# Optimization experiments

Hardware: AMD Instinct MI355X
Metric: run time of the kernel (lower is better)

Reference implementation:

```python
import jax, jax.numpy as jnp
import numpy as np

N, NS, D, HID = 8192, 512, 1024, 1024  # nodes, num_edges, f_dim, mlp hidden (max(f_dim,128))


def layernorm(x, g, b, eps=1e-5):
    m = x.mean(-1, keepdims=True)
    v = x.var(-1, keepdims=True)
    return (x - m) / jnp.sqrt(v + eps) * g + b


def mask_topk(a, kk):
    # keep only the top-kk entries of each row (vectorized version of mask_attn)
    _, idx = jax.lax.top_k(a, kk)
    rows = jnp.arange(a.shape[0])[:, None]
    mask = jnp.zeros(a.shape, a.dtype).at[rows, idx].set(1.0)
    return a * mask


def setup_inputs() -> dict:
    key = jax.random.key(0)
    ks = jax.random.split(key, 16)
    xavier = lambda k, i, o: jax.random.uniform(k, (i, o), jnp.float32, -1.0, 1.0) * np.sqrt(6.0 / (i + o))
    return {
        "inputs": jax.random.normal(ks[0], (N, D), jnp.float32),
        "noise": jax.random.normal(ks[1], (NS, D), jnp.float32),
        "edges_mu": jax.random.normal(ks[2], (1, D), jnp.float32),
        "edges_logsigma": xavier(ks[3], 1, D),
        "Wq": xavier(ks[4], D, D), "bq": jnp.zeros((D,), jnp.float32),
        "Wk": xavier(ks[5], D, D), "bk": jnp.zeros((D,), jnp.float32),
        "Wv": xavier(ks[6], D, D), "bv": jnp.zeros((D,), jnp.float32),
        "W1": xavier(ks[7], 2 * D, HID), "b1": jnp.zeros((HID,), jnp.float32),
        "W2": xavier(ks[8], HID, D), "b2": jnp.zeros((D,), jnp.float32),
        "g_in": jnp.ones((D,), jnp.float32), "b_in": jnp.zeros((D,), jnp.float32),
        "g_e": jnp.ones((D,), jnp.float32), "b_e": jnp.zeros((D,), jnp.float32),
        "k_n": 64,
        "k_e": 8,
    }


def reference(inputs, noise, edges_mu, edges_logsigma, Wq, bq, Wk, bk, Wv, bv,
              W1, b1, W2, b2, g_in, b_in, g_e, b_e, k_n, k_e):
    n, d = inputs.shape
    scale = d ** -0.5
    eps = 1e-8
    x = layernorm(inputs, g_in, b_in)                       # norm_input
    k = jax.nn.relu(x @ Wk + bk)                            # [N, D]
    v = jax.nn.relu(x @ Wv + bv)                            # [N, D]
    edges = edges_mu + jnp.exp(edges_logsigma) * noise      # [NS, D]
    # single iteration (iters=1)
    edges = layernorm(edges, g_e, b_e)                      # norm_edgs
    q = jax.nn.relu(edges @ Wq + bq)                        # [NS, D]
    dots = jnp.einsum('ni,mi->nm', q, k) * scale            # [NS, N]
    attn = jax.nn.softmax(dots, axis=1) + eps
    attn = attn / attn.sum(axis=1, keepdims=True)
    attn = mask_topk(attn, k_n)
    updates = jnp.einsum('nm,md->nd', attn, v)              # [NS, D]
    edges = jnp.concatenate([edges, updates], axis=1)       # [NS, 2D]
    edges = jax.nn.relu(edges @ W1 + b1) @ W2 + b2          # mlp -> [NS, D]
    q2 = x @ Wq + bq                                        # no relu in source
    k2 = jax.nn.relu(edges @ Wk + bk)                       # [NS, D]
    dots_v = jnp.einsum('ni,mi->nm', q2, k2) * scale        # [N, NS]
    attn_v = jax.nn.softmax(dots_v, axis=1)
    H = mask_topk(attn_v, k_e)
    return edges, H, dots
```

## Files before the change

### kernel.cpp

```cpp
#include <hip/hip_runtime.h>
#include <stdint.h>
#include <stddef.h>

typedef unsigned short u16;
typedef __bf16 bf16x8 __attribute__((ext_vector_type(8)));
typedef float f32x4 __attribute__((ext_vector_type(4)));

#define DEV __device__ __forceinline__

#define LSTR 40

DEV float bf2f(u16 u){ union{uint32_t i; float f;} c; c.i=(uint32_t)u<<16; return c.f; }
DEV u16 f2bf(float f){ union{float f; uint32_t i;} c; c.f=f; uint32_t x=c.i;
  uint32_t r = x + 0x7FFFu + ((x>>16)&1u); return (u16)(r>>16); }
DEV uint32_t fmap(float f){ union{float f; uint32_t u;} c; c.f=f;
  return (c.u & 0x80000000u) ? ~c.u : (c.u | 0x80000000u); }
DEV float funmap(uint32_t u){ union{uint32_t u; float f;} c;
  c.u = (u & 0x80000000u) ? (u & 0x7FFFFFFFu) : ~u; return c.f; }
DEV void split2(float x, u16& h, u16& l){ h = f2bf(x); l = f2bf(x - bf2f(h)); }

DEV float bredsum(float v, float* buf, int tid){
  #pragma unroll
  for(int o=32;o;o>>=1) v += __shfl_down(v,o);
  __syncthreads();
  if((tid&63)==0) buf[tid>>6]=v;
  __syncthreads();
  return buf[0]+buf[1]+buf[2]+buf[3];
}
DEV float bredmax(float v, float* buf, int tid){
  #pragma unroll
  for(int o=32;o;o>>=1) v = fmaxf(v, __shfl_down(v,o));
  __syncthreads();
  if((tid&63)==0) buf[tid>>6]=v;
  __syncthreads();
  return fmaxf(fmaxf(buf[0],buf[1]),fmaxf(buf[2],buf[3]));
}
DEV int bredsumi(int v, int* buf, int tid){
  #pragma unroll
  for(int o=32;o;o>>=1) v += __shfl_down(v,o);
  __syncthreads();
  if((tid&63)==0) buf[tid>>6]=v;
  __syncthreads();
  return buf[0]+buf[1]+buf[2]+buf[3];
}

template<bool RELU, int SK>
__global__ __launch_bounds__(256)
void gemm1_64(const u16* __restrict__ A, int lda,
              const u16* __restrict__ Bt, int ldb,
              const float* __restrict__ bias, float scale,
              u16* __restrict__ outb, float* __restrict__ outf,
              float* __restrict__ part,
              int K, int ldc, int M)
{
  __shared__ __align__(16) u16 As[64*LSTR];
  __shared__ __align__(16) u16 Bs[128*LSTR];
  const int tid = threadIdx.x, lane = tid&63, wave = tid>>6;
  const int m0 = blockIdx.y*64, n0 = blockIdx.x*128;
  const int wm = (wave>>1)*32, wn = (wave&1)*64;
  const int ml = lane&15, quad = lane>>4;
  const int srow = tid>>2, scol = (tid&3)*8;
  const int ks = K / SK;
  const int kbeg = blockIdx.z * ks;
  const u16* pa  = A  + (size_t)(m0+srow)*lda + kbeg + scol;
  const u16* pb0 = Bt + (size_t)(n0+srow)*ldb + kbeg + scol;
  const u16* pb1 = Bt + (size_t)(n0+64+srow)*ldb + kbeg + scol;

  f32x4 acc[2][4];
  #pragma unroll
  for(int i=0;i<2;i++)
    #pragma unroll
    for(int j=0;j<4;j++) acc[i][j] = (f32x4){0.f,0.f,0.f,0.f};

  uint4 ra=*(const uint4*)pa, rb0=*(const uint4*)pb0, rb1=*(const uint4*)pb1;
  for(int k0=0;k0<ks;k0+=32){
    __syncthreads();
    *(uint4*)&As[srow*LSTR + scol]      = ra;
    *(uint4*)&Bs[srow*LSTR + scol]      = rb0;
    *(uint4*)&Bs[(64+srow)*LSTR + scol] = rb1;
    __syncthreads();
    if(k0+32<ks){
      ra  = *(const uint4*)(pa +k0+32);
      rb0 = *(const uint4*)(pb0+k0+32);
      rb1 = *(const uint4*)(pb1+k0+32);
    }
    bf16x8 af[2], bf[4];
    #pragma unroll
    for(int mi=0;mi<2;mi++) af[mi] = *(const bf16x8*)&As[(wm+mi*16+ml)*LSTR + quad*8];
    #pragma unroll
    for(int ni=0;ni<4;ni++) bf[ni] = *(const bf16x8*)&Bs[(wn+ni*16+ml)*LSTR + quad*8];
    #pragma unroll
    for(int mi=0;mi<2;mi++)
      #pragma unroll
      for(int ni=0;ni<4;ni++)
        acc[mi][ni] = __builtin_amdgcn_mfma_f32_16x16x32_bf16(af[mi], bf[ni], acc[mi][ni], 0,0,0);
  }
  #pragma unroll
  for(int mi=0;mi<2;mi++){
    const int rbase = m0 + wm + mi*16 + quad*4;
    #pragma unroll
    for(int ni=0;ni<4;ni++){
      const int col = n0 + wn + ni*16 + ml;
      if(SK==1){
        const float bv = bias ? bias[col] : 0.f;
        #pragma unroll
        for(int r=0;r<4;r++){
          float v = acc[mi][ni][r]*scale + bv;
          if(RELU) v = fmaxf(v, 0.f);
          const size_t idx = (size_t)(rbase + r)*ldc + col;
          if(outb) outb[idx] = f2bf(v);
          if(outf) outf[idx] = v;
        }
      }else{
        #pragma unroll
        for(int r=0;r<4;r++)
          part[((size_t)blockIdx.z*M + rbase + r)*ldc + col] = acc[mi][ni][r];
      }
    }
  }
}

template<bool RELU, int SK>
__global__ __launch_bounds__(256)
void gemm3_64(const u16* __restrict__ Ah, const u16* __restrict__ Al, int lda,
              const u16* __restrict__ Bh, const u16* __restrict__ Bl, int ldb,
              const float* __restrict__ bias, float scale,
              u16* __restrict__ outh, u16* __restrict__ outl,
              float* __restrict__ outf, float* __restrict__ part,
              int K, int ldc, int M)
{
  __shared__ __align__(16) u16 AsH[64*LSTR];
  __shared__ __align__(16) u16 AsL[64*LSTR];
  __shared__ __align__(16) u16 BsH[128*LSTR];
  __shared__ __align__(16) u16 BsL[128*LSTR];
  const int tid = threadIdx.x, lane = tid&63, wave = tid>>6;
  const int m0 = blockIdx.y*64, n0 = blockIdx.x*128;
  const int wm = (wave>>1)*32, wn = (wave&1)*64;
  const int ml = lane&15, quad = lane>>4;
  const int srow = tid>>2, scol = (tid&3)*8;
  const int ks = K / SK;
  const int kbeg = blockIdx.z * ks;
  const size_t ao  = (size_t)(m0+srow)*lda + kbeg + scol;
  const size_t bo0 = (size_t)(n0+srow)*ldb + kbeg + scol;
  const size_t bo1 = (size_t)(n0+64+srow)*ldb + kbeg + scol;

  f32x4 acc[2][4];
  #pragma unroll
  for(int i=0;i<2;i++)
    #pragma unroll
    for(int j=0;j<4;j++) acc[i][j] = (f32x4){0.f,0.f,0.f,0.f};

  uint4 rah=*(const uint4*)(Ah+ao),  ral=*(const uint4*)(Al+ao);
  uint4 rbh0=*(const uint4*)(Bh+bo0), rbl0=*(const uint4*)(Bl+bo0);
  uint4 rbh1=*(const uint4*)(Bh+bo1), rbl1=*(const uint4*)(Bl+bo1);
  for(int k0=0;k0<ks;k0+=32){
    __syncthreads();
    *(uint4*)&AsH[srow*LSTR + scol]      = rah;
    *(uint4*)&AsL[srow*LSTR + scol]      = ral;
    *(uint4*)&BsH[srow*LSTR + scol]      = rbh0;
    *(uint4*)&BsL[srow*LSTR + scol]      = rbl0;
    *(uint4*)&BsH[(64+srow)*LSTR + scol] = rbh1;
    *(uint4*)&BsL[(64+srow)*LSTR + scol] = rbl1;
    __syncthreads();
    if(k0+32<ks){
      const int s = k0+32;
      rah =*(const uint4*)(Ah+ao +s); ral =*(const uint4*)(Al+ao +s);
      rbh0=*(const uint4*)(Bh+bo0+s); rbl0=*(const uint4*)(Bl+bo0+s);
      rbh1=*(const uint4*)(Bh+bo1+s); rbl1=*(const uint4*)(Bl+bo1+s);
    }
    bf16x8 afh[2], afl[2], bfh[4], bfl[4];
    #pragma unroll
    for(int mi=0;mi<2;mi++){
      const int o = (wm+mi*16+ml)*LSTR + quad*8;
      afh[mi] = *(const bf16x8*)&AsH[o];
      afl[mi] = *(const bf16x8*)&AsL[o];
    }
    #pragma unroll
    for(int ni=0;ni<4;ni++){
      const int o = (wn+ni*16+ml)*LSTR + quad*8;
      bfh[ni] = *(const bf16x8*)&BsH[o];
      bfl[ni] = *(const bf16x8*)&BsL[o];
    }
    #pragma unroll
    for(int mi=0;mi<2;mi++)
      #pragma unroll
      for(int ni=0;ni<4;ni++){
        acc[mi][ni] = __builtin_amdgcn_mfma_f32_16x16x32_bf16(afh[mi], bfh[ni], acc[mi][ni], 0,0,0);
        acc[mi][ni] = __builtin_amdgcn_mfma_f32_16x16x32_bf16(afh[mi], bfl[ni], acc[mi][ni], 0,0,0);
        acc[mi][ni] = __builtin_amdgcn_mfma_f32_16x16x32_bf16(afl[mi], bfh[ni], acc[mi][ni], 0,0,0);
      }
  }
  #pragma unroll
  for(int mi=0;mi<2;mi++){
    const int rbase = m0 + wm + mi*16 + quad*4;
    #pragma unroll
    for(int ni=0;ni<4;ni++){
      const int col = n0 + wn + ni*16 + ml;
      if(SK==1){
        const float bv = bias ? bias[col] : 0.f;
        #pragma unroll
        for(int r=0;r<4;r++){
          float v = acc[mi][ni][r]*scale + bv;
          if(RELU) v = fmaxf(v, 0.f);
          const size_t idx = (size_t)(rbase + r)*ldc + col;
          if(outh){ u16 h, l; split2(v, h, l); outh[idx] = h; outl[idx] = l; }
          if(outf) outf[idx] = v;
        }
      }else{
        #pragma unroll
        for(int r=0;r<4;r++)
          part[((size_t)blockIdx.z*M + rbase + r)*ldc + col] = acc[mi][ni][r];
      }
    }
  }
}

template<bool RELU, int SK>
__global__ __launch_bounds__(256)
void reduce_epi(const float* __restrict__ part, const float* __restrict__ bias,
                float scale, u16* __restrict__ outh, u16* __restrict__ outl,
                u16* __restrict__ outb, float* __restrict__ outf,
                size_t MN, int N)
{
  const size_t i = ((size_t)blockIdx.x*256 + threadIdx.x)*4;
  float4 s = *(const float4*)(part + i);
  #pragma unroll
  for(int z=1; z<SK; z++){
    const float4 t = *(const float4*)(part + (size_t)z*MN + i);
    s.x += t.x; s.y += t.y; s.z += t.z; s.w += t.w;
  }
  const int col = (int)(i % (size_t)N);
  float4 bv = bias ? *(const float4*)(bias + col) : (float4){0.f,0.f,0.f,0.f};
  float v[4] = { s.x*scale + bv.x, s.y*scale + bv.y, s.z*scale + bv.z, s.w*scale + bv.w };
  if(RELU){
    #pragma unroll
    for(int j=0;j<4;j++) v[j] = fmaxf(v[j], 0.f);
  }
  if(outh){
    ushort4 h4, l4;
    split2(v[0], h4.x, l4.x); split2(v[1], h4.y, l4.y);
    split2(v[2], h4.z, l4.z); split2(v[3], h4.w, l4.w);
    *(ushort4*)(outh + i) = h4;
    *(ushort4*)(outl + i) = l4;
  }
  if(outb){
    ushort4 b4;
    b4.x=f2bf(v[0]); b4.y=f2bf(v[1]); b4.z=f2bf(v[2]); b4.w=f2bf(v[3]);
    *(ushort4*)(outb + i) = b4;
  }
  if(outf) *(float4*)(outf + i) = (float4){v[0],v[1],v[2],v[3]};
}

__global__ __launch_bounds__(256)
void transpose_split(const float* __restrict__ in, u16* __restrict__ outh,
                     u16* __restrict__ outl, int R, int C)
{
  __shared__ float tile[32][33];
  const int tx = threadIdx.x & 31, ty = threadIdx.x >> 5;
  const int bx = blockIdx.x*32, by = blockIdx.y*32;
  #pragma unroll
  for(int i=0;i<32;i+=8)
    tile[ty+i][tx] = in[(size_t)(by+ty+i)*C + bx + tx];
  __syncthreads();
  #pragma unroll
  for(int i=0;i<32;i+=8){
    const float v = tile[tx][ty+i];
    u16 h, l; split2(v, h, l);
    const size_t o = (size_t)(bx+ty+i)*R + by + tx;
    outh[o] = h; outl[o] = l;
  }
}
__global__ __launch_bounds__(256)
void transpose_plain(const float* __restrict__ in, u16* __restrict__ outh, int R, int C)
{
  __shared__ float tile[32][33];
  const int tx = threadIdx.x & 31, ty = threadIdx.x >> 5;
  const int bx = blockIdx.x*32, by = blockIdx.y*32;
  #pragma unroll
  for(int i=0;i<32;i+=8)
    tile[ty+i][tx] = in[(size_t)(by+ty+i)*C + bx + tx];
  __syncthreads();
  #pragma unroll
  for(int i=0;i<32;i+=8)
    outh[(size_t)(bx+ty+i)*R + by + tx] = f2bf(tile[tx][ty+i]);
}
__global__ __launch_bounds__(256)
void split_convert(const float* __restrict__ in, u16* __restrict__ oh,
                   u16* __restrict__ ol)
{
  const int i = blockIdx.x*256 + threadIdx.x;
  const float4 v = ((const float4*)in)[i];
  ushort4 h4, l4;
  split2(v.x, h4.x, l4.x); split2(v.y, h4.y, l4.y);
  split2(v.z, h4.z, l4.z); split2(v.w, h4.w, l4.w);
  ((ushort4*)oh)[i] = h4; ((ushort4*)ol)[i] = l4;
}

__global__ __launch_bounds__(256)
void layernorm_rows(const float* __restrict__ in, const float* __restrict__ g,
                    const float* __restrict__ bb, u16* __restrict__ outh,
                    u16* __restrict__ outl, int ostride)
{
  __shared__ float buf[4];
  const int row = blockIdx.x, tid = threadIdx.x;
  const float4 xv = ((const float4*)(in + (size_t)row*1024))[tid];
  float s  = bredsum(xv.x+xv.y+xv.z+xv.w, buf, tid);
  float s2 = bredsum(xv.x*xv.x+xv.y*xv.y+xv.z*xv.z+xv.w*xv.w, buf, tid);
  const float mean = s * (1.f/1024.f);
  const float var  = s2 * (1.f/1024.f) - mean*mean;
  const float rs   = 1.f / sqrtf(var + 1e-5f);
  const float4 gv = ((const float4*)g)[tid];
  const float4 bv = ((const float4*)bb)[tid];
  float o0 = (xv.x-mean)*rs*gv.x + bv.x;
  float o1 = (xv.y-mean)*rs*gv.y + bv.y;
  float o2 = (xv.z-mean)*rs*gv.z + bv.z;
  float o3 = (xv.w-mean)*rs*gv.w + bv.w;
  ushort4 oh, ol;
  split2(o0, oh.x, ol.x); split2(o1, oh.y, ol.y);
  split2(o2, oh.z, ol.z); split2(o3, oh.w, ol.w);
  ((ushort4*)(outh + (size_t)row*ostride))[tid] = oh;
  ((ushort4*)(outl + (size_t)row*ostride))[tid] = ol;
}

__global__ __launch_bounds__(256)
void edges_ln(const float* __restrict__ noise, const float* __restrict__ mu,
              const float* __restrict__ lsig, const float* __restrict__ g,
              const float* __restrict__ bb, u16* __restrict__ outh,
              u16* __restrict__ outl, int ostride)
{
  __shared__ float buf[4];
  const int row = blockIdx.x, tid = threadIdx.x;
  const float4 nv  = ((const float4*)(noise + (size_t)row*1024))[tid];
  const float4 muv = ((const float4*)mu)[tid];
  const float4 lsv = ((const float4*)lsig)[tid];
  float v0 = muv.x + expf(lsv.x)*nv.x;
  float v1 = muv.y + expf(lsv.y)*nv.y;
  float v2 = muv.z + expf(lsv.z)*nv.z;
  float v3 = muv.w + expf(lsv.w)*nv.w;
  float s  = bredsum(v0+v1+v2+v3, buf, tid);
  float s2 = bredsum(v0*v0+v1*v1+v2*v2+v3*v3, buf, tid);
  const float mean = s * (1.f/1024.f);
  const float var  = s2 * (1.f/1024.f) - mean*mean;
  const float rs   = 1.f / sqrtf(var + 1e-5f);
  const float4 gv = ((const float4*)g)[tid];
  const float4 bv = ((const float4*)bb)[tid];
  float o0 = (v0-mean)*rs*gv.x + bv.x;
  float o1 = (v1-mean)*rs*gv.y + bv.y;
  float o2 = (v2-mean)*rs*gv.z + bv.z;
  float o3 = (v3-mean)*rs*gv.w + bv.w;
  ushort4 oh, ol;
  split2(o0, oh.x, ol.x); split2(o1, oh.y, ol.y);
  split2(o2, oh.z, ol.z); split2(o3, oh.w, ol.w);
  ((ushort4*)(outh + (size_t)row*ostride))[tid] = oh;
  ((ushort4*)(outl + (size_t)row*ostride))[tid] = ol;
}

#define SWZ(i) ((i) ^ (((((unsigned)(i))>>5)&7u)<<2))
__global__ __launch_bounds__(256)
void softmax_topk_a(const float* __restrict__ dots, const int* __restrict__ knp,
                    int* __restrict__ tidx, float* __restrict__ tw)
{
  const int NC = 8192;
  __shared__ __align__(16) uint32_t us[8192];
  __shared__ float fbuf[4];
  __shared__ int ibuf[4];
  __shared__ int scan[256];
  __shared__ uint32_t hist[256];
  __shared__ uint32_t bcast;
  __shared__ int slot_ctr;
  const int row = blockIdx.x, tid = threadIdx.x;
  const int lane = tid & 63, wave = tid >> 6;
  const float* x = dots + (size_t)row * NC;

  float mx = -3.4e38f;
  #pragma unroll
  for(int it=0; it<8; ++it){
    const int i = (tid + it*256)*4;
    const float4 f = *(const float4*)(x + i);
    mx = fmaxf(fmaxf(mx, fmaxf(f.x,f.y)), fmaxf(f.z,f.w));
    uint4 u; u.x=fmap(f.x); u.y=fmap(f.y); u.z=fmap(f.z); u.w=fmap(f.w);
    *(uint4*)&us[SWZ(i)] = u;
  }
  mx = bredmax(mx, fbuf, tid);

  float se = 0.f;
  #pragma unroll
  for(int it=0; it<8; ++it){
    const int i = (tid + it*256)*4;
    const uint4 u = *(const uint4*)&us[SWZ(i)];
    se += expf(funmap(u.x)-mx) + expf(funmap(u.y)-mx)
        + expf(funmap(u.z)-mx) + expf(funmap(u.w)-mx);
  }
  se = bredsum(se, fbuf, tid);
  const float T = 1.f + (float)NC * 1e-8f;

  const int k = knp[0];
  const int base = tid*32;

  uint32_t prefix = 0;
  int remaining = k;
  #pragma unroll
  for(int shift=24; shift>=0; shift-=8){
    hist[tid] = 0;
    __syncthreads();
    const uint32_t himask = (shift==24) ? 0u : (0xFFFFFFFFu << (shift+8));
    #pragma unroll
    for(int j=0;j<32;j+=4){
      const uint4 u4 = *(const uint4*)&us[SWZ(base+j)];
      const uint32_t uu[4] = {u4.x,u4.y,u4.z,u4.w};
      #pragma unroll
      for(int t=0;t<4;t++)
        if((uu[t] & himask) == prefix) atomicAdd(&hist[(uu[t]>>shift)&255u], 1u);
    }
    __syncthreads();
    if(wave==0){
      const uint32_t h0=hist[4*lane], h1=hist[4*lane+1],
                     h2=hist[4*lane+2], h3=hist[4*lane+3];
      const uint32_t s3=h3, s2=h2+s3, s1=h1+s2, s0=h0+s1;
      uint32_t tsum = s0;
      #pragma unroll
      for(int o=1;o<64;o<<=1){
        const uint32_t vv = __shfl_down(tsum, o);
        if(lane + o < 64) tsum += vv;
      }
      const uint32_t excl = tsum - s0;
      const uint32_t r = (uint32_t)remaining;
      int cand = -1; uint32_t gsel = 0;
      if     (s3+excl >= r){ cand = 4*lane+3; gsel = excl; }
      else if(s2+excl >= r){ cand = 4*lane+2; gsel = s3+excl; }
      else if(s1+excl >= r){ cand = 4*lane+1; gsel = s2+excl; }
      else if(s0+excl >= r){ cand = 4*lane+0; gsel = s1+excl; }
      int bestc = cand; uint32_t bestg = gsel;
      #pragma unroll
      for(int o=32;o;o>>=1){
        const int oc = __shfl_xor(bestc, o);
        const uint32_t og = __shfl_xor(bestg, o);
        if(oc > bestc){ bestc = oc; bestg = og; }
      }
      if(lane==0) bcast = (uint32_t)bestc;
      remaining -= (int)bestg;
    }
    __syncthreads();
    prefix |= bcast << shift;
  }
  const uint32_t uth = prefix;

  int gt = 0, eq = 0;
  #pragma unroll
  for(int j=0;j<32;j+=4){
    const uint4 u4 = *(const uint4*)&us[SWZ(base+j)];
    gt += (u4.x>uth)+(u4.y>uth)+(u4.z>uth)+(u4.w>uth);
    eq += (u4.x==uth)+(u4.y==uth)+(u4.z==uth)+(u4.w==uth);
  }
  const int c1 = bredsumi(gt, ibuf, tid);
  __syncthreads();
  scan[tid] = eq;
  __syncthreads();
  #pragma unroll
  for(int o=1;o<256;o<<=1){
    int t = (tid>=o) ? scan[tid-o] : 0;
    __syncthreads();
    scan[tid] += t;
    __syncthreads();
  }
  int eq_rank = scan[tid] - eq;
  const int budget = k - c1;
  if(tid==0) slot_ctr = 0;
  __syncthreads();
  #pragma unroll 2
  for(int j=0;j<32;j+=4){
    const uint4 u4 = *(const uint4*)&us[SWZ(base+j)];
    const uint32_t uu[4] = {u4.x,u4.y,u4.z,u4.w};
    #pragma unroll
    for(int t=0;t<4;t++){
      const uint32_t u = uu[t];
      bool sel = (u > uth);
      if(u == uth){ sel = (eq_rank < budget); eq_rank++; }
      if(sel){
        const int s = atomicAdd(&slot_ctr, 1);
        const float f = funmap(u);
        const float w = (expf(f - mx)/se + 1e-8f) / T;
        if(s < 128){ tidx[row*128 + s] = base + j + t; tw[row*128 + s] = w; }
      }
    }
  }
}

__global__ __launch_bounds__(256)
void gather_updates(const int* __restrict__ tidx, const float* __restrict__ tw,
                    const int* __restrict__ knp, const u16* __restrict__ v,
                    u16* __restrict__ cath, u16* __restrict__ catl)
{
  __shared__ int   idx_s[128];
  __shared__ float w_s[128];
  const int row = blockIdx.x, tid = threadIdx.x;
  const int kk = knp[0];
  if(tid < 128){
    idx_s[tid] = (tid < kk) ? (tidx[row*128+tid] & 8191) : 0;
    w_s[tid]   = (tid < kk) ? tw[row*128+tid] : 0.f;
  }
  __syncthreads();
  const int c = tid*4;
  float a0=0,a1=0,a2=0,a3=0;
  for(int j=0;j<kk && j<128;j++){
    const ushort4 vv = *(const ushort4*)&v[(size_t)idx_s[j]*1024 + c];
    const float w = w_s[j];
    a0 += w*bf2f(vv.x); a1 += w*bf2f(vv.y); a2 += w*bf2f(vv.z); a3 += w*bf2f(vv.w);
  }
  ushort4 oh, ol;
  split2(a0, oh.x, ol.x); split2(a1, oh.y, ol.y);
  split2(a2, oh.z, ol.z); split2(a3, oh.w, ol.w);
  ((ushort4*)(cath + (size_t)row*2048 + 1024))[tid] = oh;
  ((ushort4*)(catl + (size_t)row*2048 + 1024))[tid] = ol;
}

__global__ __launch_bounds__(256)
void bias_v_kernel(const float* __restrict__ bq, const u16* __restrict__ k2h,
                   const u16* __restrict__ k2l, float* __restrict__ out)
{
  __shared__ float buf[4];
  const int row = blockIdx.x, tid = threadIdx.x;
  const ushort4 h4 = ((const ushort4*)(k2h + (size_t)row*1024))[tid];
  const ushort4 l4 = ((const ushort4*)(k2l + (size_t)row*1024))[tid];
  const float4 b4 = ((const float4*)bq)[tid];
  float s = b4.x*(bf2f(h4.x)+bf2f(l4.x)) + b4.y*(bf2f(h4.y)+bf2f(l4.y))
          + b4.z*(bf2f(h4.z)+bf2f(l4.z)) + b4.w*(bf2f(h4.w)+bf2f(l4.w));
  s = bredsum(s, buf, tid);
  if(tid==0) out[row] = s * 0.03125f;
}

__global__ __launch_bounds__(256)
void softmax_topk_h_wave(const float* __restrict__ dv, const int* __restrict__ kep,
                         float* __restrict__ H)
{
  const int wave = threadIdx.x >> 6, lane = threadIdx.x & 63;
  const int row = blockIdx.x*4 + wave;
  const float* x = dv + (size_t)row*512 + lane*8;
  const float4 a = *(const float4*)x;
  const float4 b = *(const float4*)(x+4);
  float vals[8] = {a.x,a.y,a.z,a.w,b.x,b.y,b.z,b.w};

  float mx = vals[0];
  #pragma unroll
  for(int j=1;j<8;j++) mx = fmaxf(mx, vals[j]);
  #pragma unroll
  for(int o=32;o;o>>=1) mx = fmaxf(mx, __shfl_xor(mx, o));
  float e[8], se = 0.f;
  #pragma unroll
  for(int j=0;j<8;j++){ e[j] = expf(vals[j]-mx); se += e[j]; }
  #pragma unroll
  for(int o=32;o;o>>=1) se += __shfl_xor(se, o);
  const float inv = 1.f/se;

  const int k = kep[0];
  unsigned int selmask = 0;
  for(int r=0;r<k;r++){
    unsigned long long best = 0;
    #pragma unroll
    for(int j=0;j<8;j++){
      if(!((selmask>>j)&1u)){
        const unsigned long long key =
          ((unsigned long long)fmap(vals[j]) << 9) | (unsigned long long)(511 - (lane*8+j));
        if(key > best) best = key;
      }
    }
    #pragma unroll
    for(int o=32;o;o>>=1){
      const unsigned long long other = __shfl_xor(best, o);
      if(other > best) best = other;
    }
    const int bidx = 511 - (int)(best & 511ull);
    if((bidx>>3) == lane) selmask |= 1u << (bidx & 7);
  }

  float4 o0, o1;
  o0.x = (selmask&  1u) ? e[0]*inv : 0.f;
  o0.y = (selmask&  2u) ? e[1]*inv : 0.f;
  o0.z = (selmask&  4u) ? e[2]*inv : 0.f;
  o0.w = (selmask&  8u) ? e[3]*inv : 0.f;
  o1.x = (selmask& 16u) ? e[4]*inv : 0.f;
  o1.y = (selmask& 32u) ? e[5]*inv : 0.f;
  o1.z = (selmask& 64u) ? e[6]*inv : 0.f;
  o1.w = (selmask&128u) ? e[7]*inv : 0.f;
  float* outp = H + (size_t)row*512 + lane*8;
  *(float4*)outp     = o0;
  *(float4*)(outp+4) = o1;
}

extern "C" void kernel_launch(void* const* d_in, const int* in_sizes, int n_in,
                              void* d_out, int out_size, void* d_ws, size_t ws_size,
                              hipStream_t stream)
{
  const float* inputs = (const float*)d_in[0];
  const float* noise  = (const float*)d_in[1];
  const float* emu    = (const float*)d_in[2];
  const float* elsig  = (const float*)d_in[3];
  const float* Wq = (const float*)d_in[4];  const float* bq = (const float*)d_in[5];
  const float* Wk = (const float*)d_in[6];  const float* bk = (const float*)d_in[7];
  const float* Wv = (const float*)d_in[8];  const float* bv = (const float*)d_in[9];
  const float* W1 = (const float*)d_in[10]; const float* b1 = (const float*)d_in[11];
  const float* W2 = (const float*)d_in[12]; const float* b2 = (const float*)d_in[13];
  const float* g_in = (const float*)d_in[14]; const float* b_in = (const float*)d_in[15];
  const float* g_e  = (const float*)d_in[16]; const float* b_e  = (const float*)d_in[17];
  const int* knp = (const int*)d_in[18];
  const int* kep = (const int*)d_in[19];

  float* out = (float*)d_out;
  float* out_edges = out;
  float* out_H     = out + 512*1024;
  float* out_dots  = out + 512*1024 + 8192*512;

  char* p = (char*)d_ws;
  const size_t MB = 1024ull*1024;
  u16* xh = (u16*)(p + 0*MB);
  u16* xl = (u16*)(p + 16*MB);
  u16* kb = (u16*)(p + 32*MB);
  u16* vb = (u16*)(p + 48*MB);
  float* dotsvf = (float*)(p + 32*MB);
  u16* WkTh = (u16*)(p + 64*MB);  u16* WkTl = (u16*)(p + 66*MB);
  u16* WvTh = (u16*)(p + 68*MB);
  u16* WqTh = (u16*)(p + 70*MB);
  u16* Wqh  = (u16*)(p + 72*MB);  u16* Wql  = (u16*)(p + 74*MB);
  u16* W1Th = (u16*)(p + 76*MB);  u16* W1Tl = (u16*)(p + 80*MB);
  u16* W2Th = (u16*)(p + 84*MB);  u16* W2Tl = (u16*)(p + 86*MB);
  u16* cath = (u16*)(p + 88*MB);  u16* catl = (u16*)(p + 90*MB);
  u16* qmb  = (u16*)(p + 92*MB);
  u16* h1h  = (u16*)(p + 93*MB);  u16* h1l  = (u16*)(p + 94*MB);
  u16* eoh  = (u16*)(p + 95*MB);  u16* eol  = (u16*)(p + 96*MB);
  u16* k2h  = (u16*)(p + 97*MB);  u16* k2l  = (u16*)(p + 98*MB);
  u16* Gth  = (u16*)(p + 99*MB);  u16* Gtl  = (u16*)(p + 100*MB);
  int*   tidx  = (int*)  (p + 101*MB);
  float* tw    = (float*)(p + 101*MB + 256*1024);
  float* biasv = (float*)(p + 101*MB + 512*1024);
  float* part  = (float*)(p + 104*MB);

  hipMemsetAsync(tidx, 0, 512ull*128*4, stream);
  hipMemsetAsync(tw,   0, 512ull*128*4, stream);

  transpose_split<<<dim3(32,32),256,0,stream>>>(Wk, WkTh, WkTl, 1024, 1024);
  transpose_split<<<dim3(32,64),256,0,stream>>>(W1, W1Th, W1Tl, 2048, 1024);
  transpose_split<<<dim3(32,32),256,0,stream>>>(W2, W2Th, W2Tl, 1024, 1024);
  transpose_plain<<<dim3(32,32),256,0,stream>>>(Wv, WvTh, 1024, 1024);
  transpose_plain<<<dim3(32,32),256,0,stream>>>(Wq, WqTh, 1024, 1024);
  split_convert<<<1024,256,0,stream>>>(Wq, Wqh, Wql);

  layernorm_rows<<<8192,256,0,stream>>>(inputs, g_in, b_in, xh, xl, 1024);
  edges_ln<<<512,256,0,stream>>>(noise, emu, elsig, g_e, b_e, cath, catl, 2048);

  const size_t MN = 512ull*1024;
  gemm1_64<true,1><<<dim3(8,128),256,0,stream>>>(xh,1024, WkTh,1024, bk, 1.f,
                                                 kb,nullptr, nullptr, 1024,1024,8192);
  gemm1_64<true,1><<<dim3(8,128),256,0,stream>>>(xh,1024, WvTh,1024, bv, 1.f,
                                                 vb,nullptr, nullptr, 1024,1024,8192);
  gemm1_64<false,4><<<dim3(8,8,4),256,0,stream>>>(cath,2048, WqTh,1024, nullptr, 1.f,
                                                  nullptr,nullptr, part, 1024,1024,512);
  reduce_epi<true,4><<<512,256,0,stream>>>(part, bq, 1.f, nullptr,nullptr, qmb,nullptr, MN, 1024);
  gemm1_64<false,1><<<dim3(64,8),256,0,stream>>>(qmb,1024, kb,1024, nullptr, 0.03125f,
                                                 nullptr,out_dots, nullptr, 1024,8192,512);
  softmax_topk_a<<<512,256,0,stream>>>(out_dots, knp, tidx, tw);
  gather_updates<<<512,256,0,stream>>>(tidx, tw, knp, vb, cath, catl);

  gemm3_64<false,4><<<dim3(8,8,4),256,0,stream>>>(cath,catl,2048, W1Th,W1Tl,2048,
                                                  nullptr,1.f, nullptr,nullptr,nullptr,
                                                  part, 2048,1024,512);
  reduce_epi<true,4><<<512,256,0,stream>>>(part, b1, 1.f, h1h,h1l, nullptr,nullptr, MN, 1024);
  gemm3_64<false,4><<<dim3(8,8,4),256,0,stream>>>(h1h,h1l,1024, W2Th,W2Tl,1024,
                                                  nullptr,1.f, nullptr,nullptr,nullptr,
                                                  part, 1024,1024,512);
  reduce_epi<false,4><<<512,256,0,stream>>>(part, b2, 1.f, eoh,eol, nullptr,out_edges, MN, 1024);
  gemm3_64<false,4><<<dim3(8,8,4),256,0,stream>>>(eoh,eol,1024, WkTh,WkTl,1024,
                                                  nullptr,1.f, nullptr,nullptr,nullptr,
                                                  part, 1024,1024,512);
  reduce_epi<true,4><<<512,256,0,stream>>>(part, bk, 1.f, k2h,k2l, nullptr,nullptr, MN, 1024);
  gemm3_64<false,4><<<dim3(8,8,4),256,0,stream>>>(k2h,k2l,1024, Wqh,Wql,1024,
                                                  nullptr,1.f, nullptr,nullptr,nullptr,
                                                  part, 1024,1024,512);
  reduce_epi<false,4><<<512,256,0,stream>>>(part, nullptr, 1.f, Gth,Gtl, nullptr,nullptr, MN, 1024);
  bias_v_kernel<<<512,256,0,stream>>>(bq, k2h, k2l, biasv);
  gemm3_64<false,1><<<dim3(4,128),256,0,stream>>>(xh,xl,1024, Gth,Gtl,1024,
                                                  biasv, 0.03125f, nullptr,nullptr,dotsvf,
                                                  nullptr, 1024,512,8192);
  softmax_topk_h_wave<<<2048,256,0,stream>>>(dotsvf, kep, out_H);
}
```

Before: 416.6 us.

## Double-buffer LDS tiles in GEMM kernels with a single barrier per k-step

```diff
diff --git a/kernel.cpp b/kernel.cpp
--- a/kernel.cpp
+++ b/kernel.cpp
@@ -7,8 +7,6 @@
 typedef float f32x4 __attribute__((ext_vector_type(4)));
 
 #define DEV __device__ __forceinline__
-
-#define LSTR 40
 
 DEV float bf2f(u16 u){ union{uint32_t i; float f;} c; c.i=(uint32_t)u<<16; return c.f; }
 DEV u16 f2bf(float f){ union{float f; uint32_t i;} c; c.f=f; uint32_t x=c.i;
@@ -19,6 +17,9 @@
   c.u = (u & 0x80000000u) ? (u & 0x7FFFFFFFu) : ~u; return c.f; }
 DEV void split2(float x, u16& h, u16& l){ h = f2bf(x); l = f2bf(x - bf2f(h)); }
 
+#define LDS_BAR() do{ asm volatile("s_waitcnt lgkmcnt(0)" ::: "memory"); \
+                      __builtin_amdgcn_s_barrier(); }while(0)
+
 DEV float bredsum(float v, float* buf, int tid){
   #pragma unroll
   for(int o=32;o;o>>=1) v += __shfl_down(v,o);
@@ -53,14 +54,16 @@
               float* __restrict__ part,
               int K, int ldc, int M)
 {
-  __shared__ __align__(16) u16 As[64*LSTR];
-  __shared__ __align__(16) u16 Bs[128*LSTR];
+  __shared__ __align__(16) u16 As[2][64*32];
+  __shared__ __align__(16) u16 Bs[2][128*32];
   const int tid = threadIdx.x, lane = tid&63, wave = tid>>6;
   const int m0 = blockIdx.y*64, n0 = blockIdx.x*128;
   const int wm = (wave>>1)*32, wn = (wave&1)*64;
   const int ml = lane&15, quad = lane>>4;
   const int srow = tid>>2, scol = (tid&3)*8;
+  const int swr = srow*32 + scol;
   const int ks = K / SK;
+  const int nt = ks >> 5;
   const int kbeg = blockIdx.z * ks;
   const u16* pa  = A  + (size_t)(m0+srow)*lda + kbeg + scol;
   const u16* pb0 = Bt + (size_t)(n0+srow)*ldb + kbeg + scol;
@@ -72,28 +75,60 @@
     #pragma unroll
     for(int j=0;j<4;j++) acc[i][j] = (f32x4){0.f,0.f,0.f,0.f};
 
-  uint4 ra=*(const uint4*)pa, rb0=*(const uint4*)pb0, rb1=*(const uint4*)pb1;
-  for(int k0=0;k0<ks;k0+=32){
-    __syncthreads();
-    *(uint4*)&As[srow*LSTR + scol]      = ra;
-    *(uint4*)&Bs[srow*LSTR + scol]      = rb0;
-    *(uint4*)&Bs[(64+srow)*LSTR + scol] = rb1;
-    __syncthreads();
-    if(k0+32<ks){
-      ra  = *(const uint4*)(pa +k0+32);
-      rb0 = *(const uint4*)(pb0+k0+32);
-      rb1 = *(const uint4*)(pb1+k0+32);
-    }
-    bf16x8 af[2], bf[4];
-    #pragma unroll
-    for(int mi=0;mi<2;mi++) af[mi] = *(const bf16x8*)&As[(wm+mi*16+ml)*LSTR + quad*8];
-    #pragma unroll
-    for(int ni=0;ni<4;ni++) bf[ni] = *(const bf16x8*)&Bs[(wn+ni*16+ml)*LSTR + quad*8];
-    #pragma unroll
-    for(int mi=0;mi<2;mi++)
-      #pragma unroll
-      for(int ni=0;ni<4;ni++)
-        acc[mi][ni] = __builtin_amdgcn_mfma_f32_16x16x32_bf16(af[mi], bf[ni], acc[mi][ni], 0,0,0);
+  uint4 a0=*(const uint4*)pa, b00=*(const uint4*)pb0, b10=*(const uint4*)pb1;
+  *(uint4*)&As[0][swr]         = a0;
+  *(uint4*)&Bs[0][swr]         = b00;
+  *(uint4*)&Bs[0][64*32 + swr] = b10;
+  uint4 a1 =*(const uint4*)(pa +32);
+  uint4 b01=*(const uint4*)(pb0+32);
+  uint4 b11=*(const uint4*)(pb1+32);
+  LDS_BAR();
+
+  for(int t=0; t<nt; t+=2){
+    {
+      bf16x8 af[2], bf[4];
+      #pragma unroll
+      for(int mi=0;mi<2;mi++) af[mi] = *(const bf16x8*)&As[0][(wm+mi*16+ml)*32 + quad*8];
+      #pragma unroll
+      for(int ni=0;ni<4;ni++) bf[ni] = *(const bf16x8*)&Bs[0][(wn+ni*16+ml)*32 + quad*8];
+      *(uint4*)&As[1][swr]         = a1;
+      *(uint4*)&Bs[1][swr]         = b01;
+      *(uint4*)&Bs[1][64*32 + swr] = b11;
+      if(t+2<nt){
+        a0 =*(const uint4*)(pa +(t+2)*32);
+        b00=*(const uint4*)(pb0+(t+2)*32);
+        b10=*(const uint4*)(pb1+(t+2)*32);
+      }
+      #pragma unroll
+      for(int mi=0;mi<2;mi++)
+        #pragma unroll
+        for(int ni=0;ni<4;ni++)
+          acc[mi][ni] = __builtin_amdgcn_mfma_f32_16x16x32_bf16(af[mi], bf[ni], acc[mi][ni], 0,0,0);
+      LDS_BAR();
+    }
+    {
+      bf16x8 af[2], bf[4];
+      #pragma unroll
+      for(int mi=0;mi<2;mi++) af[mi] = *(const bf16x8*)&As[1][(wm+mi*16+ml)*32 + quad*8];
+      #pragma unroll
+      for(int ni=0;ni<4;ni++) bf[ni] = *(const bf16x8*)&Bs[1][(wn+ni*16+ml)*32 + quad*8];
+      if(t+2<nt){
+        *(uint4*)&As[0][swr]         = a0;
+        *(uint4*)&Bs[0][swr]         = b00;
+        *(uint4*)&Bs[0][64*32 + swr] = b10;
+      }
+      if(t+3<nt){
+        a1 =*(const uint4*)(pa +(t+3)*32);
+        b01=*(const uint4*)(pb0+(t+3)*32);
+        b11=*(const uint4*)(pb1+(t+3)*32);
+      }
+      #pragma unroll
+      for(int mi=0;mi<2;mi++)
+        #pragma unroll
+        for(int ni=0;ni<4;ni++)
+          acc[mi][ni] = __builtin_amdgcn_mfma_f32_16x16x32_bf16(af[mi], bf[ni], acc[mi][ni], 0,0,0);
+      LDS_BAR();
+    }
   }
   #pragma unroll
   for(int mi=0;mi<2;mi++){
@@ -129,16 +164,18 @@
               float* __restrict__ outf, float* __restrict__ part,
               int K, int ldc, int M)
 {
-  __shared__ __align__(16) u16 AsH[64*LSTR];
-  __shared__ __align__(16) u16 AsL[64*LSTR];
-  __shared__ __align__(16) u16 BsH[128*LSTR];
-  __shared__ __align__(16) u16 BsL[128*LSTR];
+  __shared__ __align__(16) u16 AsH[2][64*32];
+  __shared__ __align__(16) u16 AsL[2][64*32];
+  __shared__ __align__(16) u16 BsH[2][128*32];
+  __shared__ __align__(16) u16 BsL[2][128*32];
   const int tid = threadIdx.x, lane = tid&63, wave = tid>>6;
   const int m0 = blockIdx.y*64, n0 = blockIdx.x*128;
   const int wm = (wave>>1)*32, wn = (wave&1)*64;
   const int ml = lane&15, quad = lane>>4;
   const int srow = tid>>2, scol = (tid&3)*8;
+  const int swr = srow*32 + scol;
   const int ks = K / SK;
+  const int nt = ks >> 5;
   const int kbeg = blockIdx.z * ks;
   const size_t ao  = (size_t)(m0+srow)*lda + kbeg + scol;
   const size_t bo0 = (size_t)(n0+srow)*ldb + kbeg + scol;
@@ -150,45 +187,95 @@
     #pragma unroll
     for(int j=0;j<4;j++) acc[i][j] = (f32x4){0.f,0.f,0.f,0.f};
 
-  uint4 rah=*(const uint4*)(Ah+ao),  ral=*(const uint4*)(Al+ao);
-  uint4 rbh0=*(const uint4*)(Bh+bo0), rbl0=*(const uint4*)(Bl+bo0);
-  uint4 rbh1=*(const uint4*)(Bh+bo1), rbl1=*(const uint4*)(Bl+bo1);
-  for(int k0=0;k0<ks;k0+=32){
-    __syncthreads();
-    *(uint4*)&AsH[srow*LSTR + scol]      = rah;
-    *(uint4*)&AsL[srow*LSTR + scol]      = ral;
-    *(uint4*)&BsH[srow*LSTR + scol]      = rbh0;
-    *(uint4*)&BsL[srow*LSTR + scol]      = rbl0;
-    *(uint4*)&BsH[(64+srow)*LSTR + scol] = rbh1;
-    *(uint4*)&BsL[(64+srow)*LSTR + scol] = rbl1;
-    __syncthreads();
-    if(k0+32<ks){
-      const int s = k0+32;
-      rah =*(const uint4*)(Ah+ao +s); ral =*(const uint4*)(Al+ao +s);
-      rbh0=*(const uint4*)(Bh+bo0+s); rbl0=*(const uint4*)(Bl+bo0+s);
-      rbh1=*(const uint4*)(Bh+bo1+s); rbl1=*(const uint4*)(Bl+bo1+s);
-    }
-    bf16x8 afh[2], afl[2], bfh[4], bfl[4];
-    #pragma unroll
-    for(int mi=0;mi<2;mi++){
-      const int o = (wm+mi*16+ml)*LSTR + quad*8;
-      afh[mi] = *(const bf16x8*)&AsH[o];
-      afl[mi] = *(const bf16x8*)&AsL[o];
-    }
-    #pragma unroll
-    for(int ni=0;ni<4;ni++){
-      const int o = (wn+ni*16+ml)*LSTR + quad*8;
-      bfh[ni] = *(const bf16x8*)&BsH[o];
-      bfl[ni] = *(const bf16x8*)&BsL[o];
-    }
-    #pragma unroll
-    for(int mi=0;mi<2;mi++)
+  uint4 rah0=*(const uint4*)(Ah+ao),  ral0=*(const uint4*)(Al+ao);
+  uint4 rbh00=*(const uint4*)(Bh+bo0), rbl00=*(const uint4*)(Bl+bo0);
+  uint4 rbh10=*(const uint4*)(Bh+bo1), rbl10=*(const uint4*)(Bl+bo1);
+  *(uint4*)&AsH[0][swr]         = rah0;
+  *(uint4*)&AsL[0][swr]         = ral0;
+  *(uint4*)&BsH[0][swr]         = rbh00;
+  *(uint4*)&BsL[0][swr]         = rbl00;
+  *(uint4*)&BsH[0][64*32 + swr] = rbh10;
+  *(uint4*)&BsL[0][64*32 + swr] = rbl10;
+  uint4 rah1 =*(const uint4*)(Ah+ao +32), ral1 =*(const uint4*)(Al+ao +32);
+  uint4 rbh01=*(const uint4*)(Bh+bo0+32), rbl01=*(const uint4*)(Bl+bo0+32);
+  uint4 rbh11=*(const uint4*)(Bh+bo1+32), rbl11=*(const uint4*)(Bl+bo1+32);
+  LDS_BAR();
+
+  for(int t=0; t<nt; t+=2){
+    {
+      bf16x8 afh[2], afl[2], bfh[4], bfl[4];
+      #pragma unroll
+      for(int mi=0;mi<2;mi++){
+        const int o = (wm+mi*16+ml)*32 + quad*8;
+        afh[mi] = *(const bf16x8*)&AsH[0][o];
+        afl[mi] = *(const bf16x8*)&AsL[0][o];
+      }
       #pragma unroll
       for(int ni=0;ni<4;ni++){
-        acc[mi][ni] = __builtin_amdgcn_mfma_f32_16x16x32_bf16(afh[mi], bfh[ni], acc[mi][ni], 0,0,0);
-        acc[mi][ni] = __builtin_amdgcn_mfma_f32_16x16x32_bf16(afh[mi], bfl[ni], acc[mi][ni], 0,0,0);
-        acc[mi][ni] = __builtin_amdgcn_mfma_f32_16x16x32_bf16(afl[mi], bfh[ni], acc[mi][ni], 0,0,0);
-      }
+        const int o = (wn+ni*16+ml)*32 + quad*8;
+        bfh[ni] = *(const bf16x8*)&BsH[0][o];
+        bfl[ni] = *(const bf16x8*)&BsL[0][o];
+      }
+      *(uint4*)&AsH[1][swr]         = rah1;
+      *(uint4*)&AsL[1][swr]         = ral1;
+      *(uint4*)&BsH[1][swr]         = rbh01;
+      *(uint4*)&BsL[1][swr]         = rbl01;
+      *(uint4*)&BsH[1][64*32 + swr] = rbh11;
+      *(uint4*)&BsL[1][64*32 + swr] = rbl11;
+      if(t+2<nt){
+        const int s = (t+2)*32;
+        rah0 =*(const uint4*)(Ah+ao +s); ral0 =*(const uint4*)(Al+ao +s);
+        rbh00=*(const uint4*)(Bh+bo0+s); rbl00=*(const uint4*)(Bl+bo0+s);
+        rbh10=*(const uint4*)(Bh+bo1+s); rbl10=*(const uint4*)(Bl+bo1+s);
+      }
+      #pragma unroll
+      for(int mi=0;mi<2;mi++)
+        #pragma unroll
+        for(int ni=0;ni<4;ni++){
+          acc[mi][ni] = __builtin_amdgcn_mfma_f32_16x16x32_bf16(afh[mi], bfh[ni], acc[mi][ni], 0,0,0);
+          acc[mi][ni] = __builtin_amdgcn_mfma_f32_16x16x32_bf16(afh[mi], bfl[ni], acc[mi][ni], 0,0,0);
+          acc[mi][ni] = __builtin_amdgcn_mfma_f32_16x16x32_bf16(afl[mi], bfh[ni], acc[mi][ni], 0,0,0);
+        }
+      LDS_BAR();
+    }
+    {
+      bf16x8 afh[2], afl[2], bfh[4], bfl[4];
+      #pragma unroll
+      for(int mi=0;mi<2;mi++){
+        const int o = (wm+mi*16+ml)*32 + quad*8;
+        afh[mi] = *(const bf16x8*)&AsH[1][o];
+        afl[mi] = *(const bf16x8*)&AsL[1][o];
+      }
+      #pragma unroll
+      for(int ni=0;ni<4;ni++){
+        const int o = (wn+ni*16+ml)*32 + quad*8;
+        bfh[ni] = *(const bf16x8*)&BsH[1][o];
+        bfl[ni] = *(const bf16x8*)&BsL[1][o];
+      }
+      if(t+2<nt){
+        *(uint4*)&AsH[0][swr]         = rah0;
+        *(uint4*)&AsL[0][swr]         = ral0;
+        *(uint4*)&BsH[0][swr]         = rbh00;
+        *(uint4*)&BsL[0][swr]         = rbl00;
+        *(uint4*)&BsH[0][64*32 + swr] = rbh10;
+        *(uint4*)&BsL[0][64*32 + swr] = rbl10;
+      }
+      if(t+3<nt){
+        const int s = (t+3)*32;
+        rah1 =*(const uint4*)(Ah+ao +s); ral1 =*(const uint4*)(Al+ao +s);
+        rbh01=*(const uint4*)(Bh+bo0+s); rbl01=*(const uint4*)(Bl+bo0+s);
+        rbh11=*(const uint4*)(Bh+bo1+s); rbl11=*(const uint4*)(Bl+bo1+s);
+      }
+      #pragma unroll
+      for(int mi=0;mi<2;mi++)
+        #pragma unroll
+        for(int ni=0;ni<4;ni++){
+          acc[mi][ni] = __builtin_amdgcn_mfma_f32_16x16x32_bf16(afh[mi], bfh[ni], acc[mi][ni], 0,0,0);
+          acc[mi][ni] = __builtin_amdgcn_mfma_f32_16x16x32_bf16(afh[mi], bfl[ni], acc[mi][ni], 0,0,0);
+          acc[mi][ni] = __builtin_amdgcn_mfma_f32_16x16x32_bf16(afl[mi], bfh[ni], acc[mi][ni], 0,0,0);
+        }
+      LDS_BAR();
+    }
   }
   #pragma unroll
   for(int mi=0;mi<2;mi++){
```

Result: no change. 413.4 us (-0.8%).
